# Kernel optimization log

Measured on AMD Instinct MI355X. Metric: run time of the kernel, lower is better.

Reference implementation:

```python
import jax, jax.numpy as jnp
import numpy as np

HEADS = 8
DIM_HEAD = 32
GROUPS = 8
EPS = 1e-5


def setup_inputs() -> dict:
    key = jax.random.key(0)
    k1, k2, k3 = jax.random.split(key, 3)
    b, c, d, h, w = 1, 256, 16, 16, 16
    inner = HEADS * DIM_HEAD  # 256
    return {
        "x": jax.random.normal(k1, (b, c, d, h, w), dtype=jnp.float32),
        "gamma": jnp.ones((c,), dtype=jnp.float32),
        "beta": jnp.zeros((c,), dtype=jnp.float32),
        "w_qkv": jax.random.normal(k2, (inner * 3, c), dtype=jnp.float32) * 0.02,
        "b_qkv": jnp.zeros((inner * 3,), dtype=jnp.float32),
        "w_out": jax.random.normal(k3, (c, inner), dtype=jnp.float32) * 0.02,
        "b_out": jnp.zeros((c,), dtype=jnp.float32),
    }


def reference(x, gamma, beta, w_qkv, b_qkv, w_out, b_out):
    b, c, d, h, w = x.shape
    n = d * h * w
    # GroupNorm(8, c): normalize over (c//GROUPS, d, h, w) per group
    xg = x.reshape(b, GROUPS, c // GROUPS, n)
    mu = xg.mean(axis=(2, 3), keepdims=True)
    var = xg.var(axis=(2, 3), keepdims=True)
    xn = ((xg - mu) * jax.lax.rsqrt(var + EPS)).reshape(b, c, n)
    xn = xn * gamma[None, :, None] + beta[None, :, None]
    # 1x1 conv QKV projection (pointwise over channels)
    qkv = jnp.einsum('oc,bcn->bon', w_qkv, xn) + b_qkv[None, :, None]
    inner = HEADS * DIM_HEAD
    q, k, v = qkv[:, :inner], qkv[:, inner:2 * inner], qkv[:, 2 * inner:]
    q = q.reshape(b, HEADS, DIM_HEAD, n)  # bhdn
    k = k.reshape(b, HEADS, DIM_HEAD, n)
    v = v.reshape(b, HEADS, DIM_HEAD, n)
    scale = DIM_HEAD ** -0.5
    # full self-attention over flattened 3D volume (n = d*h*w)
    attn = jax.nn.softmax(jnp.einsum('bhdi,bhdj->bhij', q, k) * scale, axis=-1)
    out = jnp.einsum('bhij,bhdj->bhdi', attn, v).reshape(b, inner, n)
    out = jnp.einsum('oc,bcn->bon', w_out, out) + b_out[None, :, None]
    return out.reshape(b, c, d, h, w) + x
```

## Files before the change

kernel.cpp:

```cpp
#include <hip/hip_runtime.h>
#include <hip/hip_bf16.h>

#define HEADS 8
#define DIM_HEAD 32
#define GROUPS 8
#define CCH 256
#define NTOK 4096
#define EPS 1e-5f
#define GN_SPLIT 32
#define JS 4

typedef _Float16 half8 __attribute__((ext_vector_type(8)));
typedef _Float16 half4 __attribute__((ext_vector_type(4)));
typedef float f32x4 __attribute__((ext_vector_type(4)));

__global__ void gn_stats_partial(const float* __restrict__ x, float* __restrict__ part) {
    const int g  = blockIdx.y;
    const int sp = blockIdx.x;
    const int M = (CCH / GROUPS) * NTOK;
    const int chunk = M / GN_SPLIT;
    const float4* p = (const float4*)(x + (size_t)g * M + (size_t)sp * chunk);
    float s = 0.f, ss = 0.f;
    for (int i = threadIdx.x; i < chunk / 4; i += blockDim.x) {
        float4 v = p[i];
        s  += v.x + v.y + v.z + v.w;
        ss += v.x*v.x + v.y*v.y + v.z*v.z + v.w*v.w;
    }
    #pragma unroll
    for (int off = 32; off; off >>= 1) {
        s  += __shfl_down(s,  off);
        ss += __shfl_down(ss, off);
    }
    __shared__ float sh0[8], sh1[8];
    const int wave = threadIdx.x >> 6, lane = threadIdx.x & 63;
    if (lane == 0) { sh0[wave] = s; sh1[wave] = ss; }
    __syncthreads();
    if (threadIdx.x == 0) {
        float S = 0.f, SS = 0.f;
        const int nw = blockDim.x >> 6;
        for (int w = 0; w < nw; ++w) { S += sh0[w]; SS += sh1[w]; }
        part[(g * GN_SPLIT + sp) * 2]     = S;
        part[(g * GN_SPLIT + sp) * 2 + 1] = SS;
    }
}

__global__ __launch_bounds__(256)
void fold_qkv(const float* __restrict__ w, const float* __restrict__ b,
              const float* __restrict__ gamma, const float* __restrict__ beta,
              const float* __restrict__ part, const float* __restrict__ w_out,
              const float* __restrict__ x,
              _Float16* __restrict__ w2h, float* __restrict__ b2,
              _Float16* __restrict__ wouth, _Float16* __restrict__ xT) {
    const int o = blockIdx.x;
    const int c = threadIdx.x;
    if (o >= 4 * CCH) {
        const int t  = o - 4 * CCH;
        const int jb = (t & 63) * 64;
        const int cb = (t >> 6) * 64;
        __shared__ float tile[64][65];
        const int tj = threadIdx.x & 63, tc = threadIdx.x >> 6;
        #pragma unroll
        for (int cc = 0; cc < 64; cc += 4)
            tile[cc + tc][tj] = x[(size_t)(cb + cc + tc) * NTOK + jb + tj];
        __syncthreads();
        const int wc = threadIdx.x & 63, wj = threadIdx.x >> 6;
        #pragma unroll
        for (int jj = 0; jj < 64; jj += 4)
            xT[(size_t)(jb + jj + wj) * CCH + cb + wc] = (_Float16)tile[wc][jj + wj];
        return;
    }
    if (o >= 3 * CCH) {
        const int oo = o - 3 * CCH;
        wouth[(size_t)oo * CCH + c] = (_Float16)w_out[(size_t)oo * CCH + c];
        return;
    }
    __shared__ float smean[GROUPS], srstd[GROUPS];
    if (c < GROUPS) {
        float s = 0.f, ss = 0.f;
        #pragma unroll
        for (int i = 0; i < GN_SPLIT; ++i) {
            s  += part[(c * GN_SPLIT + i) * 2];
            ss += part[(c * GN_SPLIT + i) * 2 + 1];
        }
        const float M = (float)((CCH / GROUPS) * NTOK);
        const float mean = s / M;
        const float var  = ss / M - mean * mean;
        smean[c] = mean;
        srstd[c] = rsqrtf(var + EPS);
    }
    __syncthreads();
    const int g = c >> 5;
    const float sc = gamma[c] * srstd[g];
    const float sh = beta[c] - smean[g] * sc;
    const float wv = w[(size_t)o * CCH + c];
    w2h[(size_t)o * CCH + c] = (_Float16)(wv * sc);
    float t = wv * sh;
    #pragma unroll
    for (int off = 32; off; off >>= 1) t += __shfl_down(t, off);
    __shared__ float shred[4];
    const int wave = threadIdx.x >> 6, lane = threadIdx.x & 63;
    if (lane == 0) shred[wave] = t;
    __syncthreads();
    if (threadIdx.x == 0)
        b2[o] = b[o] + shred[0] + shred[1] + shred[2] + shred[3];
}

__global__ __launch_bounds__(256)
void qkv_mfma(const _Float16* __restrict__ w2h, const float* __restrict__ b2,
              const _Float16* __restrict__ xT,
              _Float16* __restrict__ q_h, _Float16* __restrict__ k_h,
              _Float16* __restrict__ vT_h) {
    const int tid = threadIdx.x, w = tid >> 6, lane = tid & 63;
    const int la = lane & 15, lg = lane >> 4;
    const int jb = blockIdx.x * 64 + w * 16;
    const int ob = blockIdx.y * 16;
    const int part = ob >> 8;
    f32x4 acc = {0.f, 0.f, 0.f, 0.f};
    if (part < 2) {
        const _Float16* arow = xT  + (size_t)(jb + la) * CCH;
        const _Float16* brow = w2h + (size_t)(ob + la) * CCH;
        #pragma unroll
        for (int kk = 0; kk < CCH; kk += 32) {
            const half8 a = *(const half8*)(arow + kk + lg * 8);
            const half8 b = *(const half8*)(brow + kk + lg * 8);
            acc = __builtin_amdgcn_mfma_f32_16x16x32_f16(a, b, acc, 0, 0, 0);
        }
        const int h = (ob & 255) >> 5, dbase = ob & 31;
        const float bias = b2[ob + la];
        _Float16* dst = (part == 0) ? q_h : k_h;
        const float scl = (part == 0) ? 0.17677669529663687f : 1.0f;
        #pragma unroll
        for (int r = 0; r < 4; ++r) {
            const int j = jb + lg * 4 + r;
            dst[((size_t)h * NTOK + j) * DIM_HEAD + dbase + la] =
                (_Float16)((acc[r] + bias) * scl);
        }
    } else {
        const _Float16* arow = w2h + (size_t)(ob + la) * CCH;
        const _Float16* brow = xT  + (size_t)(jb + la) * CCH;
        #pragma unroll
        for (int kk = 0; kk < CCH; kk += 32) {
            const half8 a = *(const half8*)(arow + kk + lg * 8);
            const half8 b = *(const half8*)(brow + kk + lg * 8);
            acc = __builtin_amdgcn_mfma_f32_16x16x32_f16(a, b, acc, 0, 0, 0);
        }
        const int h = (ob & 255) >> 5, dbase = ob & 31;
        const float4 b4 = *(const float4*)(b2 + ob + lg * 4);
        const float bb[4] = {b4.x, b4.y, b4.z, b4.w};
        #pragma unroll
        for (int r = 0; r < 4; ++r) {
            const int d = dbase + lg * 4 + r;
            vT_h[((size_t)h * DIM_HEAD + d) * NTOK + jb + la] = (_Float16)(acc[r] + bb[r]);
        }
    }
}

#define TJ 64
#define KPAD 36
#define VPAD 72
__global__ __launch_bounds__(512)
void attn_mfma(const _Float16* __restrict__ q_h, const _Float16* __restrict__ k_h,
               const _Float16* __restrict__ vT_h,
               float* __restrict__ pm, float* __restrict__ pl,
               _Float16* __restrict__ pacc) {
    const int tid = threadIdx.x;
    const int w = tid >> 6, lane = tid & 63;
    const int la = lane & 15, lg = lane >> 4;
    const int h = blockIdx.y;
    const int s = blockIdx.z;
    const int qbase = blockIdx.x * 128 + w * 16;
    const int jlen = NTOK / JS;
    const int j0 = s * jlen;

    __shared__ _Float16 lk [2][TJ * KPAD];
    __shared__ _Float16 lvt[2][DIM_HEAD * VPAD];
    __shared__ __align__(16) _Float16 plds[8][16 * 64];

    const half8 aq = *(const half8*)(q_h + ((size_t)h * NTOK + qbase + la) * DIM_HEAD + lg * 8);

    f32x4 acc0 = {0.f, 0.f, 0.f, 0.f};
    f32x4 acc1 = {0.f, 0.f, 0.f, 0.f};
    float m = -1e30f, l = 0.f;

    const _Float16* kg = k_h  + (size_t)h * NTOK * DIM_HEAD + (size_t)j0 * DIM_HEAD;
    const _Float16* vg = vT_h + (size_t)h * DIM_HEAD * NTOK + j0;
    const int krow = tid >> 3, kc8 = tid & 7;
    const int vrow = tid >> 4, vseg = tid & 15;
    char* pw = (char*)&plds[w][0];

    uint2 kreg, vreg;
    kreg = ((const uint2*)kg)[tid];
    vreg = *(const uint2*)(vg + (size_t)vrow * NTOK + vseg * 4);
    *(uint2*)&lk[0][krow * KPAD + kc8 * 4] = kreg;
    *(uint2*)&lvt[0][vrow * VPAD + vseg * 4] = vreg;
    kreg = ((const uint2*)(kg + (size_t)TJ * DIM_HEAD))[tid];
    vreg = *(const uint2*)(vg + (size_t)vrow * NTOK + TJ + vseg * 4);
    __syncthreads();

    const int NT = jlen / TJ;
    for (int t = 0; t < NT; ++t) {
        const int cur = t & 1;
        if (t + 1 < NT) {
            *(uint2*)&lk[cur ^ 1][krow * KPAD + kc8 * 4] = kreg;
            *(uint2*)&lvt[cur ^ 1][vrow * VPAD + vseg * 4] = vreg;
            if (t + 2 < NT) {
                kreg = ((const uint2*)(kg + (size_t)(t + 2) * TJ * DIM_HEAD))[tid];
                vreg = *(const uint2*)(vg + (size_t)vrow * NTOK + (t + 2) * TJ + vseg * 4);
            }
        }
        f32x4 sc[4];
        #pragma unroll
        for (int sub = 0; sub < 4; ++sub) {
            const half8 ak = *(const half8*)&lk[cur][(sub * 16 + la) * KPAD + lg * 8];
            f32x4 z = {0.f, 0.f, 0.f, 0.f};
            sc[sub] = __builtin_amdgcn_mfma_f32_16x16x32_f16(ak, aq, z, 0, 0, 0);
        }
        float tm = fmaxf(fmaxf(sc[0][0], sc[0][1]), fmaxf(sc[0][2], sc[0][3]));
        #pragma unroll
        for (int sub = 1; sub < 4; ++sub) {
            tm = fmaxf(tm, fmaxf(fmaxf(sc[sub][0], sc[sub][1]),
                                 fmaxf(sc[sub][2], sc[sub][3])));
        }
        tm = fmaxf(tm, __shfl_xor(tm, 16));
        tm = fmaxf(tm, __shfl_xor(tm, 32));
        const float mn   = fmaxf(m, tm);
        const float corr = __expf(m - mn);
        m = mn;
        l *= corr;
        #pragma unroll
        for (int r = 0; r < 4; ++r) {
            const float cq = __shfl(corr, lg * 4 + r);
            acc0[r] *= cq;
            acc1[r] *= cq;
        }
        float ps = 0.f;
        #pragma unroll
        for (int sub = 0; sub < 4; ++sub) {
            union { _Float16 hp[4]; uint2 u; } pk;
            #pragma unroll
            for (int r = 0; r < 4; ++r) {
                const float p = __expf(sc[sub][r] - mn);
                ps += p;
                pk.hp[r] = (_Float16)p;
            }
            const int unit = (sub * 2 + (lg >> 1)) ^ (la & 7);
            *(uint2*)(pw + la * 128 + unit * 16 + (lg & 1) * 8) = pk.u;
        }
        l += ps;
        #pragma unroll
        for (int kc = 0; kc < 2; ++kc) {
            const int runit = (kc * 4 + lg) ^ (la & 7);
            const half8 pa = *(const half8*)(pw + la * 128 + runit * 16);
            const half8 v0 = *(const half8*)&lvt[cur][(la     ) * VPAD + kc * 32 + lg * 8];
            const half8 v1 = *(const half8*)&lvt[cur][(la + 16) * VPAD + kc * 32 + lg * 8];
            acc0 = __builtin_amdgcn_mfma_f32_16x16x32_f16(pa, v0, acc0, 0, 0, 0);
            acc1 = __builtin_amdgcn_mfma_f32_16x16x32_f16(pa, v1, acc1, 0, 0, 0);
        }
        __syncthreads();
    }
    float lt = l;
    lt += __shfl_xor(lt, 16);
    lt += __shfl_xor(lt, 32);
    const size_t pbase = (size_t)(h * JS + s) * NTOK + qbase;
    if (lane < 16) {
        pm[pbase + la] = m;
        pl[pbase + la] = lt;
    }
    #pragma unroll
    for (int r = 0; r < 4; ++r) {
        const size_t pq = pbase + lg * 4 + r;
        pacc[pq * DIM_HEAD + la     ] = (_Float16)acc0[r];
        pacc[pq * DIM_HEAD + la + 16] = (_Float16)acc1[r];
    }
}

__global__ void attn_combine4(const float* __restrict__ pm, const float* __restrict__ pl,
                              const _Float16* __restrict__ pacc, _Float16* __restrict__ attT) {
    const int i = blockIdx.x * blockDim.x + threadIdx.x;
    const int h = blockIdx.y;
    float mv[JS], lv[JS];
    float mM = -1e30f;
    #pragma unroll
    for (int s = 0; s < JS; ++s) {
        const size_t pidx = ((size_t)(h * JS + s) * NTOK + i);
        mv[s] = pm[pidx];
        lv[s] = pl[pidx];
        mM = fmaxf(mM, mv[s]);
    }
    float wv[JS];
    float denom = 0.f;
    #pragma unroll
    for (int s = 0; s < JS; ++s) {
        wv[s] = __expf(mv[s] - mM);
        denom += lv[s] * wv[s];
    }
    const float inv = 1.f / denom;
    __attribute__((aligned(16))) _Float16 hv[DIM_HEAD];
    #pragma unroll
    for (int d0 = 0; d0 < DIM_HEAD; d0 += 4) {
        float o0 = 0.f, o1 = 0.f, o2 = 0.f, o3 = 0.f;
        #pragma unroll
        for (int s = 0; s < JS; ++s) {
            const size_t pidx = ((size_t)(h * JS + s) * NTOK + i);
            const half4 a = *(const half4*)(pacc + pidx * DIM_HEAD + d0);
            o0 = fmaf((float)a.x, wv[s], o0);
            o1 = fmaf((float)a.y, wv[s], o1);
            o2 = fmaf((float)a.z, wv[s], o2);
            o3 = fmaf((float)a.w, wv[s], o3);
        }
        hv[d0]     = (_Float16)(o0 * inv);
        hv[d0 + 1] = (_Float16)(o1 * inv);
        hv[d0 + 2] = (_Float16)(o2 * inv);
        hv[d0 + 3] = (_Float16)(o3 * inv);
    }
    _Float16* dst = attT + (size_t)i * CCH + h * DIM_HEAD;
    #pragma unroll
    for (int q = 0; q < 4; ++q) ((uint4*)dst)[q] = ((const uint4*)hv)[q];
}

__global__ __launch_bounds__(256)
void out_mfma(const _Float16* __restrict__ wouth, const float* __restrict__ bo,
              const _Float16* __restrict__ attT, const float* __restrict__ x,
              float* __restrict__ out) {
    const int tid = threadIdx.x, w = tid >> 6, lane = tid & 63;
    const int la = lane & 15, lg = lane >> 4;
    const int jb = blockIdx.x * 64 + w * 16;
    const int ob = blockIdx.y * 16;
    const _Float16* arow = wouth + (size_t)(ob + la) * CCH;
    const _Float16* brow = attT  + (size_t)(jb + la) * CCH;
    f32x4 acc = {0.f, 0.f, 0.f, 0.f};
    #pragma unroll
    for (int kk = 0; kk < CCH; kk += 32) {
        const half8 a = *(const half8*)(arow + kk + lg * 8);
        const half8 b = *(const half8*)(brow + kk + lg * 8);
        acc = __builtin_amdgcn_mfma_f32_16x16x32_f16(a, b, acc, 0, 0, 0);
    }
    const float4 b4 = *(const float4*)(bo + ob + lg * 4);
    const float bb[4] = {b4.x, b4.y, b4.z, b4.w};
    #pragma unroll
    for (int r = 0; r < 4; ++r) {
        const int o = ob + lg * 4 + r;
        const size_t idx = (size_t)o * NTOK + jb + la;
        out[idx] = acc[r] + bb[r] + x[idx];
    }
}

extern "C" void kernel_launch(void* const* d_in, const int* in_sizes, int n_in,
                              void* d_out, int out_size, void* d_ws, size_t ws_size,
                              hipStream_t stream) {
    const float* x     = (const float*)d_in[0];
    const float* gamma = (const float*)d_in[1];
    const float* beta  = (const float*)d_in[2];
    const float* w_qkv = (const float*)d_in[3];
    const float* b_qkv = (const float*)d_in[4];
    const float* w_out = (const float*)d_in[5];
    const float* b_out = (const float*)d_in[6];
    float* out = (float*)d_out;

    float* ws   = (float*)d_ws;
    float* part = ws;
    float* b2   = part + 512;
    float* pm   = b2 + 768;
    float* pl   = pm + 131072;
    _Float16* pacc = (_Float16*)(pl + 131072);
    float* fend = pl + 131072 + 2097152;
    _Float16* q_h   = (_Float16*)fend;
    _Float16* k_h   = q_h  + 1048576;
    _Float16* vT_h  = k_h  + 1048576;
    _Float16* xT    = vT_h + 1048576;
    _Float16* w2h   = xT   + 1048576;
    _Float16* wouth = w2h  + 196608;
    _Float16* attT  = wouth + 65536;

    {
        dim3 g(GN_SPLIT, GROUPS);
        gn_stats_partial<<<g, 256, 0, stream>>>(x, part);
    }
    fold_qkv<<<5 * CCH, 256, 0, stream>>>(w_qkv, b_qkv, gamma, beta, part, w_out, x,
                                          w2h, b2, wouth, xT);
    {
        dim3 g(NTOK / 64, 3 * CCH / 16);
        qkv_mfma<<<g, 256, 0, stream>>>(w2h, b2, xT, q_h, k_h, vT_h);
    }
    {
        dim3 g(NTOK / 128, HEADS, JS);
        attn_mfma<<<g, 512, 0, stream>>>(q_h, k_h, vT_h, pm, pl, pacc);
    }
    {
        dim3 g(NTOK / 256, HEADS);
        attn_combine4<<<g, 256, 0, stream>>>(pm, pl, pacc, attT);
    }
    {
        dim3 g(NTOK / 64, CCH / 16);
        out_mfma<<<g, 256, 0, stream>>>(wouth, b_out, attT, x, out);
    }
}
```

Before: 95.49 us.

## Switch attention to 32x32x16 MFMA with in-register P via permlane32 swap

Rewrites the attention kernel around 32x32x16 MFMA tiles. Each wave now covers 32 queries, and the probability matrix stays in registers, reshuffled with v_permlane32_swap instead of making a round trip through shared memory. The number of key splits doubles to 8 to keep the grid size (4096/256 × 8 heads × 8 = 1024 blocks), which grows the partial buffers and the work in the combine step. This removes the LDS stores and loads for P and the per-row correction shuffles, at the cost of larger accumulator register use.

```diff
diff --git a/kernel.cpp b/kernel.cpp
--- a/kernel.cpp
+++ b/kernel.cpp
@@ -8,11 +8,13 @@
 #define NTOK 4096
 #define EPS 1e-5f
 #define GN_SPLIT 32
-#define JS 4
+#define JS 8
 
 typedef _Float16 half8 __attribute__((ext_vector_type(8)));
 typedef _Float16 half4 __attribute__((ext_vector_type(4)));
+typedef __fp16   fp16x2 __attribute__((ext_vector_type(2)));
 typedef float f32x4 __attribute__((ext_vector_type(4)));
+typedef float f32x16 __attribute__((ext_vector_type(16)));
 
 __global__ void gn_stats_partial(const float* __restrict__ x, float* __restrict__ part) {
     const int g  = blockIdx.y;
@@ -165,35 +167,36 @@
                _Float16* __restrict__ pacc) {
     const int tid = threadIdx.x;
     const int w = tid >> 6, lane = tid & 63;
-    const int la = lane & 15, lg = lane >> 4;
+    const int la32 = lane & 31, hi = lane >> 5;
     const int h = blockIdx.y;
     const int s = blockIdx.z;
-    const int qbase = blockIdx.x * 128 + w * 16;
+    const int qbase = blockIdx.x * 256 + w * 32;
     const int jlen = NTOK / JS;
     const int j0 = s * jlen;
 
     __shared__ _Float16 lk [2][TJ * KPAD];
     __shared__ _Float16 lvt[2][DIM_HEAD * VPAD];
-    __shared__ __align__(16) _Float16 plds[8][16 * 64];
-
-    const half8 aq = *(const half8*)(q_h + ((size_t)h * NTOK + qbase + la) * DIM_HEAD + lg * 8);
-
-    f32x4 acc0 = {0.f, 0.f, 0.f, 0.f};
-    f32x4 acc1 = {0.f, 0.f, 0.f, 0.f};
+
+    const _Float16* qrow = q_h + ((size_t)h * NTOK + qbase + la32) * DIM_HEAD;
+    const half8 bq0 = *(const half8*)(qrow + hi * 8);
+    const half8 bq1 = *(const half8*)(qrow + 16 + hi * 8);
+
+    f32x16 acc;
+    #pragma unroll
+    for (int r = 0; r < 16; ++r) acc[r] = 0.f;
     float m = -1e30f, l = 0.f;
 
-    const _Float16* kg = k_h  + (size_t)h * NTOK * DIM_HEAD + (size_t)j0 * DIM_HEAD;
-    const _Float16* vg = vT_h + (size_t)h * DIM_HEAD * NTOK + j0;
+    const _Float16* kg_ = k_h  + (size_t)h * NTOK * DIM_HEAD + (size_t)j0 * DIM_HEAD;
+    const _Float16* vg  = vT_h + (size_t)h * DIM_HEAD * NTOK + j0;
     const int krow = tid >> 3, kc8 = tid & 7;
     const int vrow = tid >> 4, vseg = tid & 15;
-    char* pw = (char*)&plds[w][0];
 
     uint2 kreg, vreg;
-    kreg = ((const uint2*)kg)[tid];
+    kreg = ((const uint2*)kg_)[tid];
     vreg = *(const uint2*)(vg + (size_t)vrow * NTOK + vseg * 4);
     *(uint2*)&lk[0][krow * KPAD + kc8 * 4] = kreg;
     *(uint2*)&lvt[0][vrow * VPAD + vseg * 4] = vreg;
-    kreg = ((const uint2*)(kg + (size_t)TJ * DIM_HEAD))[tid];
+    kreg = ((const uint2*)(kg_ + (size_t)TJ * DIM_HEAD))[tid];
     vreg = *(const uint2*)(vg + (size_t)vrow * NTOK + TJ + vseg * 4);
     __syncthreads();
 
@@ -204,78 +207,79 @@
             *(uint2*)&lk[cur ^ 1][krow * KPAD + kc8 * 4] = kreg;
             *(uint2*)&lvt[cur ^ 1][vrow * VPAD + vseg * 4] = vreg;
             if (t + 2 < NT) {
-                kreg = ((const uint2*)(kg + (size_t)(t + 2) * TJ * DIM_HEAD))[tid];
+                kreg = ((const uint2*)(kg_ + (size_t)(t + 2) * TJ * DIM_HEAD))[tid];
                 vreg = *(const uint2*)(vg + (size_t)vrow * NTOK + (t + 2) * TJ + vseg * 4);
             }
         }
-        f32x4 sc[4];
-        #pragma unroll
-        for (int sub = 0; sub < 4; ++sub) {
-            const half8 ak = *(const half8*)&lk[cur][(sub * 16 + la) * KPAD + lg * 8];
-            f32x4 z = {0.f, 0.f, 0.f, 0.f};
-            sc[sub] = __builtin_amdgcn_mfma_f32_16x16x32_f16(ak, aq, z, 0, 0, 0);
-        }
-        float tm = fmaxf(fmaxf(sc[0][0], sc[0][1]), fmaxf(sc[0][2], sc[0][3]));
-        #pragma unroll
-        for (int sub = 1; sub < 4; ++sub) {
-            tm = fmaxf(tm, fmaxf(fmaxf(sc[sub][0], sc[sub][1]),
-                                 fmaxf(sc[sub][2], sc[sub][3])));
-        }
-        tm = fmaxf(tm, __shfl_xor(tm, 16));
+        f32x16 z;
+        #pragma unroll
+        for (int r = 0; r < 16; ++r) z[r] = 0.f;
+        const half8 ak00 = *(const half8*)&lk[cur][(la32     ) * KPAD +      hi * 8];
+        const half8 ak01 = *(const half8*)&lk[cur][(la32     ) * KPAD + 16 + hi * 8];
+        const half8 ak10 = *(const half8*)&lk[cur][(32 + la32) * KPAD +      hi * 8];
+        const half8 ak11 = *(const half8*)&lk[cur][(32 + la32) * KPAD + 16 + hi * 8];
+        f32x16 sc0 = __builtin_amdgcn_mfma_f32_32x32x16_f16(ak00, bq0, z, 0, 0, 0);
+        sc0        = __builtin_amdgcn_mfma_f32_32x32x16_f16(ak01, bq1, sc0, 0, 0, 0);
+        f32x16 sc1 = __builtin_amdgcn_mfma_f32_32x32x16_f16(ak10, bq0, z, 0, 0, 0);
+        sc1        = __builtin_amdgcn_mfma_f32_32x32x16_f16(ak11, bq1, sc1, 0, 0, 0);
+        float tm = sc0[0];
+        #pragma unroll
+        for (int r = 1; r < 16; ++r) tm = fmaxf(tm, sc0[r]);
+        #pragma unroll
+        for (int r = 0; r < 16; ++r) tm = fmaxf(tm, sc1[r]);
         tm = fmaxf(tm, __shfl_xor(tm, 32));
         const float mn   = fmaxf(m, tm);
         const float corr = __expf(m - mn);
         m = mn;
         l *= corr;
         #pragma unroll
-        for (int r = 0; r < 4; ++r) {
-            const float cq = __shfl(corr, lg * 4 + r);
-            acc0[r] *= cq;
-            acc1[r] *= cq;
-        }
+        for (int r = 0; r < 16; ++r) acc[r] *= corr;
+        float p0[16], p1[16];
         float ps = 0.f;
         #pragma unroll
-        for (int sub = 0; sub < 4; ++sub) {
-            union { _Float16 hp[4]; uint2 u; } pk;
-            #pragma unroll
-            for (int r = 0; r < 4; ++r) {
-                const float p = __expf(sc[sub][r] - mn);
-                ps += p;
-                pk.hp[r] = (_Float16)p;
-            }
-            const int unit = (sub * 2 + (lg >> 1)) ^ (la & 7);
-            *(uint2*)(pw + la * 128 + unit * 16 + (lg & 1) * 8) = pk.u;
-        }
+        for (int r = 0; r < 16; ++r) { p0[r] = __expf(sc0[r] - mn); ps += p0[r]; }
+        #pragma unroll
+        for (int r = 0; r < 16; ++r) { p1[r] = __expf(sc1[r] - mn); ps += p1[r]; }
         l += ps;
-        #pragma unroll
-        for (int kc = 0; kc < 2; ++kc) {
-            const int runit = (kc * 4 + lg) ^ (la & 7);
-            const half8 pa = *(const half8*)(pw + la * 128 + runit * 16);
-            const half8 v0 = *(const half8*)&lvt[cur][(la     ) * VPAD + kc * 32 + lg * 8];
-            const half8 v1 = *(const half8*)&lvt[cur][(la + 16) * VPAD + kc * 32 + lg * 8];
-            acc0 = __builtin_amdgcn_mfma_f32_16x16x32_f16(pa, v0, acc0, 0, 0, 0);
-            acc1 = __builtin_amdgcn_mfma_f32_16x16x32_f16(pa, v1, acc1, 0, 0, 0);
-        }
+        #define DO_CHUNK(P, C2, CIDX)                                              \
+        {                                                                          \
+            union { fp16x2 hh; unsigned u; } A_, B_, C_, D_;                       \
+            A_.hh = __builtin_amdgcn_cvt_pkrtz(P[8*(C2)+0], P[8*(C2)+1]);          \
+            B_.hh = __builtin_amdgcn_cvt_pkrtz(P[8*(C2)+2], P[8*(C2)+3]);          \
+            C_.hh = __builtin_amdgcn_cvt_pkrtz(P[8*(C2)+4], P[8*(C2)+5]);          \
+            D_.hh = __builtin_amdgcn_cvt_pkrtz(P[8*(C2)+6], P[8*(C2)+7]);          \
+            asm("v_permlane32_swap_b32 %0, %1" : "+v"(A_.u), "+v"(C_.u));          \
+            asm("v_permlane32_swap_b32 %0, %1" : "+v"(B_.u), "+v"(D_.u));          \
+            union { unsigned u[4]; half8 v; } F_;                                  \
+            F_.u[0] = A_.u; F_.u[1] = B_.u; F_.u[2] = C_.u; F_.u[3] = D_.u;        \
+            const half8 av = *(const half8*)&lvt[cur][la32 * VPAD + (CIDX) * 16 + hi * 8]; \
+            acc = __builtin_amdgcn_mfma_f32_32x32x16_f16(av, F_.v, acc, 0, 0, 0);  \
+        }
+        DO_CHUNK(p0, 0, 0)
+        DO_CHUNK(p0, 1, 1)
+        DO_CHUNK(p1, 0, 2)
+        DO_CHUNK(p1, 1, 3)
+        #undef DO_CHUNK
         __syncthreads();
     }
-    float lt = l;
-    lt += __shfl_xor(lt, 16);
-    lt += __shfl_xor(lt, 32);
+    float lt = l + __shfl_xor(l, 32);
     const size_t pbase = (size_t)(h * JS + s) * NTOK + qbase;
-    if (lane < 16) {
-        pm[pbase + la] = m;
-        pl[pbase + la] = lt;
-    }
-    #pragma unroll
-    for (int r = 0; r < 4; ++r) {
-        const size_t pq = pbase + lg * 4 + r;
-        pacc[pq * DIM_HEAD + la     ] = (_Float16)acc0[r];
-        pacc[pq * DIM_HEAD + la + 16] = (_Float16)acc1[r];
-    }
-}
-
-__global__ void attn_combine4(const float* __restrict__ pm, const float* __restrict__ pl,
-                              const _Float16* __restrict__ pacc, _Float16* __restrict__ attT) {
+    if (hi == 0) {
+        pm[pbase + la32] = m;
+        pl[pbase + la32] = lt;
+    }
+    #pragma unroll
+    for (int g = 0; g < 4; ++g) {
+        union { fp16x2 hh; unsigned u; } u0, u1;
+        u0.hh = __builtin_amdgcn_cvt_pkrtz(acc[4*g],     acc[4*g + 1]);
+        u1.hh = __builtin_amdgcn_cvt_pkrtz(acc[4*g + 2], acc[4*g + 3]);
+        uint2 st; st.x = u0.u; st.y = u1.u;
+        *(uint2*)(pacc + (pbase + la32) * DIM_HEAD + 8 * g + 4 * hi) = st;
+    }
+}
+
+__global__ void attn_combine(const float* __restrict__ pm, const float* __restrict__ pl,
+                             const _Float16* __restrict__ pacc, _Float16* __restrict__ attT) {
     const int i = blockIdx.x * blockDim.x + threadIdx.x;
     const int h = blockIdx.y;
     float mv[JS], lv[JS];
@@ -361,9 +365,9 @@
     float* part = ws;
     float* b2   = part + 512;
     float* pm   = b2 + 768;
-    float* pl   = pm + 131072;
-    _Float16* pacc = (_Float16*)(pl + 131072);
-    float* fend = pl + 131072 + 2097152;
+    float* pl   = pm + 262144;
+    _Float16* pacc = (_Float16*)(pl + 262144);
+    float* fend = pl + 262144 + 4194304;
     _Float16* q_h   = (_Float16*)fend;
     _Float16* k_h   = q_h  + 1048576;
     _Float16* vT_h  = k_h  + 1048576;
@@ -383,12 +387,12 @@
         qkv_mfma<<<g, 256, 0, stream>>>(w2h, b2, xT, q_h, k_h, vT_h);
     }
     {
-        dim3 g(NTOK / 128, HEADS, JS);
+        dim3 g(NTOK / 256, HEADS, JS);
         attn_mfma<<<g, 512, 0, stream>>>(q_h, k_h, vT_h, pm, pl, pacc);
     }
     {
         dim3 g(NTOK / 256, HEADS);
-        attn_combine4<<<g, 256, 0, stream>>>(pm, pl, pacc, attT);
+        attn_combine<<<g, 256, 0, stream>>>(pm, pl, pacc, attT);
     }
     {
         dim3 g(NTOK / 64, CCH / 16);
```

Result: faster. 88.94 us (-6.9%).
